# Kernel tuning notes

Measured on AMD Instinct MI355X. Metric: run time of the kernel, lower is better.

## Reference

```python
import jax, jax.numpy as jnp
import numpy as np

H = 256          # hidden size per direction (lstm_hdn_size // 2)
EPS = 1e-5       # BatchNorm1d eps


def _lstm_cell_step(x, w_ih, w_hh, b_ih, b_hh):
    # Single-timestep LSTM cell with zero initial (h, c). seq_len == 1 so both
    # directions reduce to one cell step. x: [N, in], w_ih: [4H, in], w_hh: [4H, H]
    h0 = jnp.zeros((x.shape[0], H), x.dtype)
    gates = x @ w_ih.T + b_ih + h0 @ w_hh.T + b_hh   # [N, 4H], torch gate order i,f,g,o
    i, f, g, o = jnp.split(gates, 4, axis=-1)
    c = jax.nn.sigmoid(i) * jnp.tanh(g)              # f * c0 == 0
    h = jax.nn.sigmoid(o) * jnp.tanh(c)
    return h


def _emission(x, bn_gamma, bn_beta, w_ih_l0, w_hh_l0, b_ih_l0, b_hh_l0,
              w_ih_l1, w_hh_l1, b_ih_l1, b_hh_l1, fc_w, fc_b):
    # x: [N, 1, D]; BatchNorm1d over channel D, training-mode batch statistics
    mu = jnp.mean(x, axis=(0, 1))
    var = jnp.var(x, axis=(0, 1))
    b = (x - mu) * jax.lax.rsqrt(var + EPS) * bn_gamma + bn_beta
    b = b[:, 0, :]                                   # squeeze seq_len == 1 -> [N, D]
    # bidirectional layer 0 (both directions see the same single timestep)
    h0f = _lstm_cell_step(b, w_ih_l0[0], w_hh_l0[0], b_ih_l0[0], b_hh_l0[0])
    h0b = _lstm_cell_step(b, w_ih_l0[1], w_hh_l0[1], b_ih_l0[1], b_hh_l0[1])
    h1_in = jnp.concatenate([h0f, h0b], axis=-1)     # [N, 2H]
    # bidirectional layer 1 (inter-layer LSTM dropout = identity in eval)
    h1f = _lstm_cell_step(h1_in, w_ih_l1[0], w_hh_l1[0], b_ih_l1[0], b_hh_l1[0])
    h1b = _lstm_cell_step(h1_in, w_ih_l1[1], w_hh_l1[1], b_ih_l1[1], b_hh_l1[1])
    h = jnp.concatenate([h1f, h1b], axis=-1)         # [N, 2H]
    # Dropout(p) is identity in eval; fc1 -> 2 tags
    return h @ fc_w.T + fc_b                          # [N, 2]


def _crf_nll(e, tags, crf_start, crf_end, crf_trans):
    # torchcrf CRF negative log-likelihood, chain length N, batch 1, full mask.
    # e: [N, 2], tags: [N]
    N = e.shape[0]
    num = (crf_start[tags[0]] + jnp.sum(e[jnp.arange(N), tags])
           + jnp.sum(crf_trans[tags[:-1], tags[1:]]) + crf_end[tags[-1]])
    def step(alpha, et):
        alpha = jax.nn.logsumexp(alpha[:, None] + crf_trans, axis=0) + et
        return alpha, None
    alpha0 = crf_start + e[0]
    alphaN, _ = jax.lax.scan(step, alpha0, e[1:])
    den = jax.nn.logsumexp(alphaN + crf_end)
    return -(num - den)                               # loss = -crf(emissions, tags)


def setup_inputs():
    key = jax.random.key(0)
    ks = jax.random.split(key, 16)
    N, D = 65536, 768
    s = 0.05
    return {
        "x": jax.random.normal(ks[0], (N, 1, D), jnp.float32),
        "bn_gamma": jnp.ones((D,), jnp.float32),
        "bn_beta": jnp.zeros((D,), jnp.float32),
        "w_ih_l0": jax.random.normal(ks[1], (2, 4 * H, D), jnp.float32) * s,
        "w_hh_l0": jax.random.normal(ks[2], (2, 4 * H, H), jnp.float32) * s,
        "b_ih_l0": jax.random.normal(ks[3], (2, 4 * H), jnp.float32) * s,
        "b_hh_l0": jax.random.normal(ks[4], (2, 4 * H), jnp.float32) * s,
        "w_ih_l1": jax.random.normal(ks[5], (2, 4 * H, 2 * H), jnp.float32) * s,
        "w_hh_l1": jax.random.normal(ks[6], (2, 4 * H, H), jnp.float32) * s,
        "b_ih_l1": jax.random.normal(ks[7], (2, 4 * H), jnp.float32) * s,
        "b_hh_l1": jax.random.normal(ks[8], (2, 4 * H), jnp.float32) * s,
        "fc_w": jax.random.normal(ks[9], (2, 2 * H), jnp.float32) * s,
        "fc_b": jnp.zeros((2,), jnp.float32),
        "crf_start": jax.random.normal(ks[10], (2,), jnp.float32) * s,
        "crf_end": jax.random.normal(ks[11], (2,), jnp.float32) * s,
        "crf_trans": jax.random.normal(ks[12], (2, 2), jnp.float32) * s,
        "labels": jax.random.randint(ks[13], (N,), 0, 2),
    }


def reference(x, bn_gamma, bn_beta, w_ih_l0, w_hh_l0, b_ih_l0, b_hh_l0,
              w_ih_l1, w_hh_l1, b_ih_l1, b_hh_l1, fc_w, fc_b,
              crf_start, crf_end, crf_trans, labels):
    e = _emission(x, bn_gamma, bn_beta, w_ih_l0, w_hh_l0, b_ih_l0, b_hh_l0,
                  w_ih_l1, w_hh_l1, b_ih_l1, b_hh_l1, fc_w, fc_b)
    loss = _crf_nll(e, labels, crf_start, crf_end, crf_trans)
    logits = e[:, None, :]   # [N, 1, 2], matches torch `emission`
    return loss, logits
```

## Files before the change

kernel.cpp:

```cpp
#include <hip/hip_runtime.h>

typedef _Float16 f16x8 __attribute__((ext_vector_type(8)));
typedef _Float16 f16x4 __attribute__((ext_vector_type(4)));
typedef float f32x4 __attribute__((ext_vector_type(4)));

static constexpr int NROWS = 65536;

static constexpr size_t OB_BG0  = 0;
static constexpr size_t OB_BG1  = OB_BG0 + 6144;
static constexpr size_t OB_W1H  = OB_BG1 + 6144;
static constexpr size_t OB_W1L  = OB_W1H + 2359296;
static constexpr size_t OB_W2H  = OB_W1L + 2359296;
static constexpr size_t OB_W2L  = OB_W2H + 1572864;
static constexpr size_t OB_E    = OB_W2L + 1572864;
static constexpr size_t OB_PMAT = OB_E + 524288;
static constexpr size_t OB_NUM  = OB_PMAT + 16384;
static constexpr size_t OB_H    = OB_NUM + 256;
static constexpr size_t OB_PSUM  = OB_H;
static constexpr size_t OB_PSUM2 = OB_PSUM + 786432;
static constexpr size_t OB_SF    = OB_PSUM2 + 786432;
static constexpr size_t OB_TF    = OB_SF + 3072;

__device__ __forceinline__ float sigm_(float x) { return 1.f / (1.f + __expf(-x)); }
__device__ __forceinline__ float tanh_(float x) {
  x = fminf(fmaxf(x, -15.f), 15.f);
  float e = __expf(2.f * x);
  return (e - 1.f) / (e + 1.f);
}
__device__ __forceinline__ float lse2_(float a, float b) {
  float m = fmaxf(a, b);
  float d = fabsf(a - b);
  return m + log1pf(expf(-d));
}
__device__ __forceinline__ void gload16(const void* g, void* l) {
  __builtin_amdgcn_global_load_lds(
      (const __attribute__((address_space(1))) void*)g,
      (__attribute__((address_space(3))) void*)l, 16, 0, 0);
}

__device__ __forceinline__ size_t wf_off(int q, int k, int K) {
  return ((size_t)(q >> 4) * (K >> 5) + (k >> 5)) * 512 +
         (size_t)(((k >> 3) & 3) * 128 + (q & 15) * 8 + (k & 7));
}

__global__ __launch_bounds__(256) void bn_partial(const float* __restrict__ x,
                                                  float* __restrict__ psum,
                                                  float* __restrict__ psum2) {
  int d = blockIdx.x * 256 + threadIdx.x;
  int chunk = blockIdx.y;
  const float* p = x + (size_t)chunk * 256 * 768 + d;
  float s = 0.f, s2 = 0.f;
  #pragma unroll 8
  for (int r = 0; r < 256; ++r) {
    float v = p[(size_t)r * 768];
    s += v;
    s2 = fmaf(v, v, s2);
  }
  psum[(size_t)chunk * 768 + d] = s;
  psum2[(size_t)chunk * 768 + d] = s2;
}

__global__ __launch_bounds__(256) void bn_finalize(const float* __restrict__ gamma,
                                                   const float* __restrict__ beta,
                                                   const float* __restrict__ psum,
                                                   const float* __restrict__ psum2,
                                                   float* __restrict__ sf_out,
                                                   float* __restrict__ tf_out) {
  int d = blockIdx.x * 256 + threadIdx.x;
  float s = 0.f, s2 = 0.f;
  for (int c = 0; c < 256; ++c) {
    s  += psum[(size_t)c * 768 + d];
    s2 += psum2[(size_t)c * 768 + d];
  }
  float mu  = s  * (1.f / NROWS);
  float var = s2 * (1.f / NROWS) - mu * mu;
  float sf  = rsqrtf(var + 1e-5f) * gamma[d];
  sf_out[d] = sf;
  tf_out[d] = beta[d] - mu * sf;
}

__global__ __launch_bounds__(256) void prep_w0(const float* __restrict__ w,
                                               const float* __restrict__ b_ih,
                                               const float* __restrict__ b_hh,
                                               const float* __restrict__ sf,
                                               const float* __restrict__ tf,
                                               _Float16* __restrict__ wh,
                                               _Float16* __restrict__ wl,
                                               float* __restrict__ bg) {
  int q = blockIdx.x;
  int s = q >> 9, j = q & 511, dir = j >> 8, jj = j & 255;
  int goff = (s == 0) ? 0 : ((s == 1) ? 512 : 768);
  int row = dir * 1024 + goff + jj;
  const float* src = w + (size_t)row * 768;
  float acc = 0.f;
  for (int d = threadIdx.x; d < 768; d += 256) {
    float wv = src[d];
    float wf = wv * sf[d];
    _Float16 h = (_Float16)wf;
    size_t o = wf_off(q, d, 768);
    wh[o] = h;
    wl[o] = (_Float16)(wf - (float)h);
    acc = fmaf(wv, tf[d], acc);
  }
  for (int off = 32; off; off >>= 1) acc += __shfl_down(acc, off);
  __shared__ float red[4];
  if ((threadIdx.x & 63) == 0) red[threadIdx.x >> 6] = acc;
  __syncthreads();
  if (threadIdx.x == 0)
    bg[q] = red[0] + red[1] + red[2] + red[3] + b_ih[row] + b_hh[row];
}

__global__ __launch_bounds__(256) void prep_w1(const float* __restrict__ w,
                                               const float* __restrict__ b_ih,
                                               const float* __restrict__ b_hh,
                                               _Float16* __restrict__ wh,
                                               _Float16* __restrict__ wl,
                                               float* __restrict__ bg) {
  int q = blockIdx.x;
  int s = q >> 9, j = q & 511, dir = j >> 8, jj = j & 255;
  int goff = (s == 0) ? 0 : ((s == 1) ? 512 : 768);
  int row = dir * 1024 + goff + jj;
  const float* src = w + (size_t)row * 512;
  for (int d = threadIdx.x; d < 512; d += 256) {
    float wv = src[d];
    _Float16 h = (_Float16)wv;
    size_t o = wf_off(q, d, 512);
    wh[o] = h;
    wl[o] = (_Float16)(wv - (float)h);
  }
  if (threadIdx.x == 0) bg[q] = b_ih[row] + b_hh[row];
}

__global__ __launch_bounds__(256) void init_misc(const float* __restrict__ fc_b,
                                                 float* __restrict__ e,
                                                 float* __restrict__ num) {
  int i = blockIdx.x * 256 + threadIdx.x;
  if (i < NROWS * 2) e[i] = fc_b[i & 1];
  if (i == 0) num[0] = 0.f;
}

__device__ __forceinline__ void mfma_step(const char* AhB, const char* AlB,
                                          const char* BhB, const char* BlB,
                                          int lane16, int wm, int wc,
                                          f32x4 acc[4][3][2]) {
  #pragma unroll
  for (int kk = 0; kk < 2; ++kk) {
    f16x8 ah[4], al[4];
    #pragma unroll
    for (int mf = 0; mf < 4; ++mf) {
      int ln = ((wm * 4 + mf) * 2 + kk) * 1024 + lane16;
      ah[mf] = *(const f16x8*)(AhB + ln);
      al[mf] = *(const f16x8*)(AlB + ln);
    }
    #pragma unroll
    for (int s = 0; s < 3; ++s)
      #pragma unroll
      for (int jf = 0; jf < 2; ++jf) {
        int ln = ((s * 4 + wc * 2 + jf) * 2 + kk) * 1024 + lane16;
        f16x8 bh = *(const f16x8*)(BhB + ln);
        f16x8 bl = *(const f16x8*)(BlB + ln);
        #pragma unroll
        for (int mf = 0; mf < 4; ++mf) {
          acc[mf][s][jf] = __builtin_amdgcn_mfma_f32_16x16x32_f16(ah[mf], bh, acc[mf][s][jf], 0, 0, 0);
          acc[mf][s][jf] = __builtin_amdgcn_mfma_f32_16x16x32_f16(ah[mf], bl, acc[mf][s][jf], 0, 0, 0);
          acc[mf][s][jf] = __builtin_amdgcn_mfma_f32_16x16x32_f16(al[mf], bh, acc[mf][s][jf], 0, 0, 0);
        }
      }
  }
}

template <int K>
__device__ __forceinline__ void stage_A(const float* __restrict__ Arow0,
                                        int k0, int tid,
                                        char* AhB, char* AlB) {
  #pragma unroll
  for (int p = 0; p < 4; ++p) {
    int idx = p * 256 + tid;
    int row = idx >> 3, ks = idx & 7;
    const float* src = Arow0 + (size_t)row * K + k0 + ks * 8;
    const float4 v0 = *(const float4*)src;
    const float4 v1 = *(const float4*)(src + 4);
    f16x8 hv, lv;
    hv[0] = (_Float16)v0.x; lv[0] = (_Float16)(v0.x - (float)hv[0]);
    hv[1] = (_Float16)v0.y; lv[1] = (_Float16)(v0.y - (float)hv[1]);
    hv[2] = (_Float16)v0.z; lv[2] = (_Float16)(v0.z - (float)hv[2]);
    hv[3] = (_Float16)v0.w; lv[3] = (_Float16)(v0.w - (float)hv[3]);
    hv[4] = (_Float16)v1.x; lv[4] = (_Float16)(v1.x - (float)hv[4]);
    hv[5] = (_Float16)v1.y; lv[5] = (_Float16)(v1.y - (float)hv[5]);
    hv[6] = (_Float16)v1.z; lv[6] = (_Float16)(v1.z - (float)hv[6]);
    hv[7] = (_Float16)v1.w; lv[7] = (_Float16)(v1.w - (float)hv[7]);
    int waddr = ((row >> 4) * 2 + (ks >> 2)) * 1024 + (ks & 3) * 256 + (row & 15) * 16;
    *(f16x8*)(AhB + waddr) = hv;
    *(f16x8*)(AlB + waddr) = lv;
  }
}

template <int K>
__device__ __forceinline__ void stage_B(const _Float16* __restrict__ Wh,
                                        const _Float16* __restrict__ Wl,
                                        int c0, int k0, int wvid, int lane,
                                        char* BhB, char* BlB) {
  const int lane8 = lane * 8;
  #pragma unroll
  for (int it = 0; it < 6; ++it) {
    int l24 = wvid + it * 4;
    int kh = l24 & 1, srb = l24 >> 1;
    int s = srb >> 2, rb = srb & 3;
    int grb = s * 32 + (c0 >> 4) + rb;
    size_t src = ((size_t)grb * (K >> 5) + (k0 >> 5) + kh) * 512 + lane8;
    gload16(Wh + src, BhB + l24 * 1024);
    gload16(Wl + src, BlB + l24 * 1024);
  }
}

__global__ __launch_bounds__(256, 2) void gemm1(const float* __restrict__ A,
                                                const _Float16* __restrict__ Wh,
                                                const _Float16* __restrict__ Wl,
                                                const float* __restrict__ bg,
                                                float* __restrict__ H) {
  constexpr int K = 768;
  __shared__ __align__(16) char AhB[16384], AlB[16384];
  __shared__ __align__(16) char BhB[24576], BlB[24576];

  const int tid = threadIdx.x;
  const int lane = tid & 63, wvid = tid >> 6;
  const int l15 = lane & 15, lhi = lane >> 4;
  const int wm = wvid >> 1, wc = wvid & 1;
  const int lane16 = lane * 16;

  int bid = blockIdx.y * 8 + blockIdx.x;
  int wid = (bid & 7) * 512 + (bid >> 3);
  const int m0 = (wid >> 3) * 128;
  const int c0 = (wid & 7) * 64;
  const float* Arow0 = A + (size_t)m0 * K;

  f32x4 acc[4][3][2] = {};

  for (int k0 = 0; k0 < K; k0 += 64) {
    stage_B<K>(Wh, Wl, c0, k0, wvid, lane, BhB, BlB);
    stage_A<K>(Arow0, k0, tid, AhB, AlB);
    __syncthreads();
    mfma_step(AhB, AlB, BhB, BlB, lane16, wm, wc, acc);
    __syncthreads();
  }

  const int rb = m0 + wm * 64 + lhi * 4;
  #pragma unroll
  for (int mf = 0; mf < 4; ++mf)
    #pragma unroll
    for (int jf = 0; jf < 2; ++jf) {
      const int hcol = c0 + wc * 32 + jf * 16 + l15;
      const float bi = bg[hcol], bgv = bg[512 + hcol], bo = bg[1024 + hcol];
      #pragma unroll
      for (int r = 0; r < 4; ++r) {
        float gi = acc[mf][0][jf][r] + bi;
        float gg = acc[mf][1][jf][r] + bgv;
        float go = acc[mf][2][jf][r] + bo;
        float cv = sigm_(gi) * tanh_(gg);
        H[(size_t)(rb + mf * 16 + r) * 512 + hcol] = sigm_(go) * tanh_(cv);
      }
    }
}

__global__ __launch_bounds__(256, 2) void gemm2(const float* __restrict__ A,
                                                const _Float16* __restrict__ Wh,
                                                const _Float16* __restrict__ Wl,
                                                const float* __restrict__ bg,
                                                const float* __restrict__ fcw,
                                                float* __restrict__ ew) {
  constexpr int K = 512;
  __shared__ __align__(16) char AhB[16384], AlB[16384];
  __shared__ __align__(16) char BhB[24576], BlB[24576];

  const int tid = threadIdx.x;
  const int lane = tid & 63, wvid = tid >> 6;
  const int l15 = lane & 15, lhi = lane >> 4;
  const int wm = wvid >> 1, wc = wvid & 1;
  const int lane16 = lane * 16;

  int bid = blockIdx.y * 8 + blockIdx.x;
  int wid = (bid & 7) * 512 + (bid >> 3);
  const int m0 = (wid >> 3) * 128;
  const int c0 = (wid & 7) * 64;
  const float* Arow0 = A + (size_t)m0 * K;

  f32x4 acc[4][3][2] = {};

  for (int k0 = 0; k0 < K; k0 += 64) {
    stage_B<K>(Wh, Wl, c0, k0, wvid, lane, BhB, BlB);
    stage_A<K>(Arow0, k0, tid, AhB, AlB);
    __syncthreads();
    mfma_step(AhB, AlB, BhB, BlB, lane16, wm, wc, acc);
    __syncthreads();
  }

  const int rb = m0 + wm * 64 + lhi * 4;
  #pragma unroll
  for (int mf = 0; mf < 4; ++mf) {
    float pe0[4] = {0.f, 0.f, 0.f, 0.f}, pe1[4] = {0.f, 0.f, 0.f, 0.f};
    #pragma unroll
    for (int jf = 0; jf < 2; ++jf) {
      const int hcol = c0 + wc * 32 + jf * 16 + l15;
      const float bi = bg[hcol], bgv = bg[512 + hcol], bo = bg[1024 + hcol];
      const float f0 = fcw[hcol], f1 = fcw[512 + hcol];
      #pragma unroll
      for (int r = 0; r < 4; ++r) {
        float gi = acc[mf][0][jf][r] + bi;
        float gg = acc[mf][1][jf][r] + bgv;
        float go = acc[mf][2][jf][r] + bo;
        float cv = sigm_(gi) * tanh_(gg);
        float h  = sigm_(go) * tanh_(cv);
        pe0[r] = fmaf(h, f0, pe0[r]);
        pe1[r] = fmaf(h, f1, pe1[r]);
      }
    }
    #pragma unroll
    for (int r = 0; r < 4; ++r) {
      float a0 = pe0[r], a1 = pe1[r];
      #pragma unroll
      for (int off = 1; off < 16; off <<= 1) {
        a0 += __shfl_xor(a0, off);
        a1 += __shfl_xor(a1, off);
      }
      if (l15 == 0) {
        int rowg = rb + mf * 16 + r;
        atomicAdd(&ew[(size_t)rowg * 2 + 0], a0);
        atomicAdd(&ew[(size_t)rowg * 2 + 1], a1);
      }
    }
  }
}

__global__ __launch_bounds__(256) void crf_partial(const float* __restrict__ ew,
                                                   const int* __restrict__ labels,
                                                   const float* __restrict__ trans,
                                                   float* __restrict__ pmat,
                                                   float* __restrict__ numacc) {
  int g = blockIdx.x * 256 + threadIdx.x;
  int t0 = 1 + g * 64;
  int t1 = t0 + 64; if (t1 > NROWS) t1 = NROWS;
  const float t00 = trans[0], t01 = trans[1], t10 = trans[2], t11 = trans[3];
  float p00 = 0.f, p01 = -1e30f, p10 = -1e30f, p11 = 0.f;
  float num = 0.f;
  int prev = labels[t0 - 1];
  for (int t = t0; t < t1; ++t) {
    float e0 = ew[(size_t)t * 2], e1 = ew[(size_t)t * 2 + 1];
    float m00 = t00 + e0, m01 = t01 + e1, m10 = t10 + e0, m11 = t11 + e1;
    float n00 = lse2_(p00 + m00, p01 + m10);
    float n01 = lse2_(p00 + m01, p01 + m11);
    float n10 = lse2_(p10 + m00, p11 + m10);
    float n11 = lse2_(p10 + m01, p11 + m11);
    p00 = n00; p01 = n01; p10 = n10; p11 = n11;
    int cur = labels[t];
    num += (cur ? e1 : e0) + trans[prev * 2 + cur];
    prev = cur;
  }
  float* pm = pmat + (size_t)g * 4;
  pm[0] = p00; pm[1] = p01; pm[2] = p10; pm[3] = p11;
  for (int off = 32; off; off >>= 1) num += __shfl_down(num, off);
  if ((threadIdx.x & 63) == 0) atomicAdd(numacc, num);
}

__global__ __launch_bounds__(256) void crf_final(const float* __restrict__ ew,
                                                 const int* __restrict__ labels,
                                                 const float* __restrict__ cstart,
                                                 const float* __restrict__ cend,
                                                 const float* __restrict__ pmat,
                                                 const float* __restrict__ numacc,
                                                 float* __restrict__ out) {
  __shared__ float sm[256][4];
  int t = threadIdx.x;
  const float* pm = pmat + (size_t)t * 16;
  float p00 = pm[0], p01 = pm[1], p10 = pm[2], p11 = pm[3];
  #pragma unroll
  for (int u = 1; u < 4; ++u) {
    const float* q = pm + u * 4;
    float b00 = q[0], b01 = q[1], b10 = q[2], b11 = q[3];
    float n00 = lse2_(p00 + b00, p01 + b10);
    float n01 = lse2_(p00 + b01, p01 + b11);
    float n10 = lse2_(p10 + b00, p11 + b10);
    float n11 = lse2_(p10 + b01, p11 + b11);
    p00 = n00; p01 = n01; p10 = n10; p11 = n11;
  }
  sm[t][0] = p00; sm[t][1] = p01; sm[t][2] = p10; sm[t][3] = p11;
  __syncthreads();
  for (int s = 1; s < 256; s <<= 1) {
    int i = t * (s << 1);
    if (i + s < 256) {
      float a00 = sm[i][0], a01 = sm[i][1], a10 = sm[i][2], a11 = sm[i][3];
      float b00 = sm[i + s][0], b01 = sm[i + s][1], b10 = sm[i + s][2], b11 = sm[i + s][3];
      sm[i][0] = lse2_(a00 + b00, a01 + b10);
      sm[i][1] = lse2_(a00 + b01, a01 + b11);
      sm[i][2] = lse2_(a10 + b00, a11 + b10);
      sm[i][3] = lse2_(a10 + b01, a11 + b11);
    }
    __syncthreads();
  }
  if (t == 0) {
    float a0 = cstart[0] + ew[0];
    float a1 = cstart[1] + ew[1];
    float aN0 = lse2_(a0 + sm[0][0], a1 + sm[0][2]);
    float aN1 = lse2_(a0 + sm[0][1], a1 + sm[0][3]);
    float den = lse2_(aN0 + cend[0], aN1 + cend[1]);
    int tag0 = labels[0], tagN = labels[NROWS - 1];
    float num = numacc[0] + cstart[tag0] + ew[tag0] + cend[tagN];
    out[0] = den - num;
  }
}

__global__ __launch_bounds__(256) void copy_logits(const float* __restrict__ ew,
                                                   float* __restrict__ out) {
  int i = blockIdx.x * 256 + threadIdx.x;
  if (i < NROWS * 2) out[1 + i] = ew[i];
}

extern "C" void kernel_launch(void* const* d_in, const int* in_sizes, int n_in,
                              void* d_out, int out_size, void* d_ws, size_t ws_size,
                              hipStream_t stream) {
  const float* x        = (const float*)d_in[0];
  const float* gamma    = (const float*)d_in[1];
  const float* beta     = (const float*)d_in[2];
  const float* w_ih_l0  = (const float*)d_in[3];
  const float* b_ih_l0  = (const float*)d_in[5];
  const float* b_hh_l0  = (const float*)d_in[6];
  const float* w_ih_l1  = (const float*)d_in[7];
  const float* b_ih_l1  = (const float*)d_in[9];
  const float* b_hh_l1  = (const float*)d_in[10];
  const float* fc_w     = (const float*)d_in[11];
  const float* fc_b     = (const float*)d_in[12];
  const float* crf_start= (const float*)d_in[13];
  const float* crf_end  = (const float*)d_in[14];
  const float* crf_trans= (const float*)d_in[15];
  const int*   labels   = (const int*)d_in[16];

  char* ws   = (char*)d_ws;
  float* out = (float*)d_out;

  float*     bg0  = (float*)(ws + OB_BG0);
  float*     bg1  = (float*)(ws + OB_BG1);
  _Float16*  w1h  = (_Float16*)(ws + OB_W1H);
  _Float16*  w1l  = (_Float16*)(ws + OB_W1L);
  _Float16*  w2h  = (_Float16*)(ws + OB_W2H);
  _Float16*  w2l  = (_Float16*)(ws + OB_W2L);
  float*     e    = (float*)(ws + OB_E);
  float*     pmat = (float*)(ws + OB_PMAT);
  float*     num  = (float*)(ws + OB_NUM);
  float*     H    = (float*)(ws + OB_H);
  float*     psum = (float*)(ws + OB_PSUM);
  float*     psum2= (float*)(ws + OB_PSUM2);
  float*     sf   = (float*)(ws + OB_SF);
  float*     tf   = (float*)(ws + OB_TF);

  bn_partial<<<dim3(3, 256), 256, 0, stream>>>(x, psum, psum2);
  bn_finalize<<<3, 256, 0, stream>>>(gamma, beta, psum, psum2, sf, tf);
  prep_w0<<<1536, 256, 0, stream>>>(w_ih_l0, b_ih_l0, b_hh_l0, sf, tf, w1h, w1l, bg0);
  prep_w1<<<1536, 256, 0, stream>>>(w_ih_l1, b_ih_l1, b_hh_l1, w2h, w2l, bg1);
  init_misc<<<512, 256, 0, stream>>>(fc_b, e, num);

  gemm1<<<dim3(8, 512), 256, 0, stream>>>(x, w1h, w1l, bg0, H);
  gemm2<<<dim3(8, 512), 256, 0, stream>>>(H, w2h, w2l, bg1, fc_w, e);

  crf_partial<<<4, 256, 0, stream>>>(e, labels, crf_trans, pmat, num);
  crf_final<<<1, 256, 0, stream>>>(e, labels, crf_start, crf_end, pmat, num, out);
  copy_logits<<<512, 256, 0, stream>>>(e, out);
}
```

Measured before the change: 1.346 ms.

## Store hidden layer as pre-split fp16 hi/lo in MFMA fragment layout

gemm1's epilogue now writes the hidden activations as two fp16 arrays (high and low residual parts) laid out in the MFMA fragment order, instead of fp32 row-major. gemm2 then stages A with direct global-to-LDS loads rather than loading fp32 and splitting in registers, which removes the conversion ALU work and the register round trip from gemm2's inner loop. gemm1's A staging also reorders the thread-to-row mapping. The cost is scattered 2-byte stores in gemm1's epilogue, while the total bytes of the intermediate stay the same.

```diff
diff --git a/kernel.cpp b/kernel.cpp
--- a/kernel.cpp
+++ b/kernel.cpp
@@ -1,7 +1,6 @@
 #include <hip/hip_runtime.h>
 
 typedef _Float16 f16x8 __attribute__((ext_vector_type(8)));
-typedef _Float16 f16x4 __attribute__((ext_vector_type(4)));
 typedef float f32x4 __attribute__((ext_vector_type(4)));
 
 static constexpr int NROWS = 65536;
@@ -15,8 +14,9 @@
 static constexpr size_t OB_E    = OB_W2L + 1572864;
 static constexpr size_t OB_PMAT = OB_E + 524288;
 static constexpr size_t OB_NUM  = OB_PMAT + 16384;
-static constexpr size_t OB_H    = OB_NUM + 256;
-static constexpr size_t OB_PSUM  = OB_H;
+static constexpr size_t OB_HH   = OB_NUM + 256;
+static constexpr size_t OB_HL   = OB_HH + 67108864;
+static constexpr size_t OB_PSUM  = OB_HH;
 static constexpr size_t OB_PSUM2 = OB_PSUM + 786432;
 static constexpr size_t OB_SF    = OB_PSUM2 + 786432;
 static constexpr size_t OB_TF    = OB_SF + 3072;
@@ -38,9 +38,9 @@
       (__attribute__((address_space(3))) void*)l, 16, 0, 0);
 }
 
-__device__ __forceinline__ size_t wf_off(int q, int k, int K) {
-  return ((size_t)(q >> 4) * (K >> 5) + (k >> 5)) * 512 +
-         (size_t)(((k >> 3) & 3) * 128 + (q & 15) * 8 + (k & 7));
+__device__ __forceinline__ size_t frag_off(int row, int k, int K) {
+  return ((size_t)(row >> 4) * (K >> 5) + (k >> 5)) * 512 +
+         (size_t)(((k >> 3) & 3) * 128 + (row & 15) * 8 + (k & 7));
 }
 
 __global__ __launch_bounds__(256) void bn_partial(const float* __restrict__ x,
@@ -97,7 +97,7 @@
     float wv = src[d];
     float wf = wv * sf[d];
     _Float16 h = (_Float16)wf;
-    size_t o = wf_off(q, d, 768);
+    size_t o = frag_off(q, d, 768);
     wh[o] = h;
     wl[o] = (_Float16)(wf - (float)h);
     acc = fmaf(wv, tf[d], acc);
@@ -124,7 +124,7 @@
   for (int d = threadIdx.x; d < 512; d += 256) {
     float wv = src[d];
     _Float16 h = (_Float16)wv;
-    size_t o = wf_off(q, d, 512);
+    size_t o = frag_off(q, d, 512);
     wh[o] = h;
     wl[o] = (_Float16)(wv - (float)h);
   }
@@ -170,14 +170,16 @@
 }
 
 template <int K>
-__device__ __forceinline__ void stage_A(const float* __restrict__ Arow0,
-                                        int k0, int tid,
-                                        char* AhB, char* AlB) {
+__device__ __forceinline__ void stage_A_split(const float* __restrict__ Arow0,
+                                              int k0, int tid,
+                                              char* AhB, char* AlB) {
   #pragma unroll
   for (int p = 0; p < 4; ++p) {
     int idx = p * 256 + tid;
-    int row = idx >> 3, ks = idx & 7;
-    const float* src = Arow0 + (size_t)row * K + k0 + ks * 8;
+    int row15 = idx & 15;
+    int ks    = (idx >> 4) & 7;
+    int rowg  = idx >> 7;
+    const float* src = Arow0 + (size_t)(rowg * 16 + row15) * K + k0 + ks * 8;
     const float4 v0 = *(const float4*)src;
     const float4 v1 = *(const float4*)(src + 4);
     f16x8 hv, lv;
@@ -189,9 +191,24 @@
     hv[5] = (_Float16)v1.y; lv[5] = (_Float16)(v1.y - (float)hv[5]);
     hv[6] = (_Float16)v1.z; lv[6] = (_Float16)(v1.z - (float)hv[6]);
     hv[7] = (_Float16)v1.w; lv[7] = (_Float16)(v1.w - (float)hv[7]);
-    int waddr = ((row >> 4) * 2 + (ks >> 2)) * 1024 + (ks & 3) * 256 + (row & 15) * 16;
+    int waddr = (rowg * 2 + (ks >> 2)) * 1024 + (ks & 3) * 256 + row15 * 16;
     *(f16x8*)(AhB + waddr) = hv;
     *(f16x8*)(AlB + waddr) = lv;
+  }
+}
+
+__device__ __forceinline__ void stage_A_gl(const _Float16* __restrict__ Hh,
+                                           const _Float16* __restrict__ Hl,
+                                           int m0, int k0, int wvid, int lane,
+                                           char* AhB, char* AlB) {
+  const int lane8 = lane * 8;
+  #pragma unroll
+  for (int it = 0; it < 4; ++it) {
+    int blk = wvid + it * 4;
+    int rowg = blk >> 1, kk = blk & 1;
+    size_t src = (((size_t)(m0 >> 4) + rowg) * 16 + (k0 >> 5) + kk) * 512 + lane8;
+    gload16(Hh + src, AhB + blk * 1024);
+    gload16(Hl + src, AlB + blk * 1024);
   }
 }
 
@@ -217,7 +234,8 @@
                                                 const _Float16* __restrict__ Wh,
                                                 const _Float16* __restrict__ Wl,
                                                 const float* __restrict__ bg,
-                                                float* __restrict__ H) {
+                                                _Float16* __restrict__ Hh,
+                                                _Float16* __restrict__ Hl) {
   constexpr int K = 768;
   __shared__ __align__(16) char AhB[16384], AlB[16384];
   __shared__ __align__(16) char BhB[24576], BlB[24576];
@@ -238,7 +256,7 @@
 
   for (int k0 = 0; k0 < K; k0 += 64) {
     stage_B<K>(Wh, Wl, c0, k0, wvid, lane, BhB, BlB);
-    stage_A<K>(Arow0, k0, tid, AhB, AlB);
+    stage_A_split<K>(Arow0, k0, tid, AhB, AlB);
     __syncthreads();
     mfma_step(AhB, AlB, BhB, BlB, lane16, wm, wc, acc);
     __syncthreads();
@@ -251,18 +269,26 @@
     for (int jf = 0; jf < 2; ++jf) {
       const int hcol = c0 + wc * 32 + jf * 16 + l15;
       const float bi = bg[hcol], bgv = bg[512 + hcol], bo = bg[1024 + hcol];
+      const int cpart = ((hcol >> 3) & 3) * 128 + (hcol & 7);
+      const size_t cblk = (size_t)(hcol >> 5);
       #pragma unroll
       for (int r = 0; r < 4; ++r) {
+        int m = rb + mf * 16 + r;
         float gi = acc[mf][0][jf][r] + bi;
         float gg = acc[mf][1][jf][r] + bgv;
         float go = acc[mf][2][jf][r] + bo;
         float cv = sigm_(gi) * tanh_(gg);
-        H[(size_t)(rb + mf * 16 + r) * 512 + hcol] = sigm_(go) * tanh_(cv);
+        float h  = sigm_(go) * tanh_(cv);
+        size_t o = ((size_t)(m >> 4) * 16 + cblk) * 512 + cpart + (m & 15) * 8;
+        _Float16 h16 = (_Float16)h;
+        Hh[o] = h16;
+        Hl[o] = (_Float16)(h - (float)h16);
       }
     }
 }
 
-__global__ __launch_bounds__(256, 2) void gemm2(const float* __restrict__ A,
+__global__ __launch_bounds__(256, 2) void gemm2(const _Float16* __restrict__ Hh,
+                                                const _Float16* __restrict__ Hl,
                                                 const _Float16* __restrict__ Wh,
                                                 const _Float16* __restrict__ Wl,
                                                 const float* __restrict__ bg,
@@ -282,13 +308,12 @@
   int wid = (bid & 7) * 512 + (bid >> 3);
   const int m0 = (wid >> 3) * 128;
   const int c0 = (wid & 7) * 64;
-  const float* Arow0 = A + (size_t)m0 * K;
 
   f32x4 acc[4][3][2] = {};
 
   for (int k0 = 0; k0 < K; k0 += 64) {
+    stage_A_gl(Hh, Hl, m0, k0, wvid, lane, AhB, AlB);
     stage_B<K>(Wh, Wl, c0, k0, wvid, lane, BhB, BlB);
-    stage_A<K>(Arow0, k0, tid, AhB, AlB);
     __syncthreads();
     mfma_step(AhB, AlB, BhB, BlB, lane16, wm, wc, acc);
     __syncthreads();
@@ -445,7 +470,8 @@
   float*     e    = (float*)(ws + OB_E);
   float*     pmat = (float*)(ws + OB_PMAT);
   float*     num  = (float*)(ws + OB_NUM);
-  float*     H    = (float*)(ws + OB_H);
+  _Float16*  hh   = (_Float16*)(ws + OB_HH);
+  _Float16*  hl   = (_Float16*)(ws + OB_HL);
   float*     psum = (float*)(ws + OB_PSUM);
   float*     psum2= (float*)(ws + OB_PSUM2);
   float*     sf   = (float*)(ws + OB_SF);
@@ -457,8 +483,8 @@
   prep_w1<<<1536, 256, 0, stream>>>(w_ih_l1, b_ih_l1, b_hh_l1, w2h, w2l, bg1);
   init_misc<<<512, 256, 0, stream>>>(fc_b, e, num);
 
-  gemm1<<<dim3(8, 512), 256, 0, stream>>>(x, w1h, w1l, bg0, H);
-  gemm2<<<dim3(8, 512), 256, 0, stream>>>(H, w2h, w2l, bg1, fc_w, e);
+  gemm1<<<dim3(8, 512), 256, 0, stream>>>(x, w1h, w1l, bg0, hh, hl);
+  gemm2<<<dim3(8, 512), 256, 0, stream>>>(hh, hl, w2h, w2l, bg1, fc_w, e);
 
   crf_partial<<<4, 256, 0, stream>>>(e, labels, crf_trans, pmat, num);
   crf_final<<<1, 256, 0, stream>>>(e, labels, crf_start, crf_end, pmat, num, out);
```

Result: faster. 1.207 ms (-10.3%).
